# Kernel optimization log

Measured on AMD Instinct MI355X. Metric: run time of the kernel, lower is better.

## Reference

```python
import jax, jax.numpy as jnp
import numpy as np

NUM_HEADS = 16
NUM_GROUPS = 4
NUM_KV_HEADS = NUM_HEADS // NUM_GROUPS  # 4
HEAD_DIM = 64
MAX_DIST = 484


def setup_inputs() -> dict:
    key = jax.random.key(0)
    ks = jax.random.split(key, 8)
    B, S, E, H = 32, 484, 1024, 1024
    kv_dim = HEAD_DIM * NUM_GROUPS  # 256
    s_in = 0.03
    return {
        "query": jax.random.normal(ks[0], (B, S, E), dtype=jnp.float32),
        "key": jax.random.normal(ks[1], (B, S, E), dtype=jnp.float32),
        "value": jax.random.normal(ks[2], (B, S, E), dtype=jnp.float32),
        "Wq": jax.random.normal(ks[3], (E, H), dtype=jnp.float32) * s_in,
        "Wk": jax.random.normal(ks[4], (E, kv_dim), dtype=jnp.float32) * s_in,
        "Wv": jax.random.normal(ks[5], (E, kv_dim), dtype=jnp.float32) * s_in,
        "Wo": jax.random.normal(ks[6], (H, E), dtype=jnp.float32) * s_in,
        "rel_table": jax.random.normal(ks[7], (2 * MAX_DIST - 1, NUM_HEADS), dtype=jnp.float32) * 0.02,
    }


def _rel_bias(rel_table, q_len, k_len):
    # relative position k - q, clipped to [-(MD-1), MD-1], shifted to table index
    rel = jnp.arange(k_len)[None, :] - jnp.arange(q_len)[:, None]
    idx = jnp.clip(rel, -(MAX_DIST - 1), MAX_DIST - 1) + (MAX_DIST - 1)
    bias = rel_table[idx]  # [q, k, heads]
    return jnp.transpose(bias, (2, 0, 1))  # [heads, q, k]


def reference(query, key, value, Wq, Wk, Wv, Wo, rel_table):
    B, Q, _ = query.shape
    K = key.shape[1]
    G, Hkv, D = NUM_GROUPS, NUM_KV_HEADS, HEAD_DIM
    # projections; torch head split: head index = g*Hkv + h
    q = (query @ Wq).reshape(B, Q, G * Hkv, D).transpose(0, 2, 1, 3)
    q = q.reshape(B, G, Hkv, Q, D)  # b g h sq d
    k = (key @ Wk).reshape(B, K, G, D).transpose(0, 2, 1, 3)  # b g sk d
    v = (value @ Wv).reshape(B, K, G, D).transpose(0, 2, 1, 3)  # b g sv d
    scale = jnp.float32(D) ** 0.5
    scores = jnp.einsum('bghqd,bgkd->bghqk', q, k) / scale
    bias = _rel_bias(rel_table, Q, K).reshape(1, G, Hkv, Q, K)
    attn = jax.nn.softmax(scores + bias, axis=-1)
    out = jnp.einsum('bghqk,bgkd->bghqd', attn, v)
    out = out.reshape(B, G * Hkv, Q, D).transpose(0, 2, 1, 3).reshape(B, Q, G * Hkv * D)
    return out @ Wo
```

## Files before the change

kernel.cpp:

```cpp
#include <hip/hip_runtime.h>
#include <hip/hip_bf16.h>

typedef __attribute__((ext_vector_type(8))) short short8;
typedef __attribute__((ext_vector_type(4))) float f32x4;

#define B_  32
#define S_  484
#define E_  1024
#define NH  16
#define SP  512
#define M_  (B_*S_)

static __device__ __forceinline__ ushort f2bf(float f) {
  union { float f; unsigned u; } v; v.f = f;
  unsigned u = v.u;
  return (ushort)((u + 0x7FFFu + ((u >> 16) & 1u)) >> 16);
}

#define GLOAD_LDS16(gp, lp) \
  __builtin_amdgcn_global_load_lds((const __attribute__((address_space(1))) void*)(gp), \
                                   (__attribute__((address_space(3))) void*)(lp), 16, 0, 0)

__global__ __launch_bounds__(256)
void cvt_f32_bf16(const float* __restrict__ x, ushort* __restrict__ y, int n4) {
  int i = blockIdx.x * 256 + threadIdx.x;
  int stride = gridDim.x * 256;
  for (; i < n4; i += stride) {
    float4 v = ((const float4*)x)[i];
    ushort4 h;
    h.x = f2bf(v.x); h.y = f2bf(v.y); h.z = f2bf(v.z); h.w = f2bf(v.w);
    ((ushort4*)y)[i] = h;
  }
}

__global__ __launch_bounds__(256)
void transpose_convert(const float* __restrict__ W, ushort* __restrict__ WT, int K, int N) {
  __shared__ float tile[32][33];
  int k0 = blockIdx.y * 32, n0 = blockIdx.x * 32;
  int tx = threadIdx.x, ty = threadIdx.y;
  for (int i = ty; i < 32; i += 8) tile[i][tx] = W[(size_t)(k0 + i) * N + n0 + tx];
  __syncthreads();
  for (int i = ty; i < 32; i += 8) WT[(size_t)(n0 + i) * K + k0 + tx] = f2bf(tile[tx][i]);
}

template<int EPI, int SWZ>
__global__ __launch_bounds__(256)
void gemm_bt(const ushort* __restrict__ A, const ushort* __restrict__ BT,
             void* __restrict__ Cout, int N, int K, int HN, float oscale) {
  __shared__ alignas(16) ushort sA[2][128 * 32];
  __shared__ alignas(16) ushort sB[2][128 * 32];
  const int tid = threadIdx.x;
  const int lane = tid & 63, w = tid >> 6;
  const int m0 = blockIdx.y * 128, n0 = blockIdx.x * 128;
  const int NK = K >> 5;

  const int srow = w * 32 + (lane >> 2);
  const int scol = (lane & 3) * 8;
  const ushort* gA0 = A  + (size_t)(m0 + srow) * K + scol;
  const ushort* gB0 = BT + (size_t)(n0 + srow) * K + scol;

  const int wr = w >> 1, wc = w & 1;
  const int g4 = lane >> 4, l16 = lane & 15;
  const int aoff = (wr * 64 + l16) * 32 + 8 * g4;
  const int boff = (wc * 64 + l16) * 32 + 8 * g4;

  f32x4 acc[4][4] = {};

  {
    const ushort* ga = gA0; const ushort* gb = gB0;
    GLOAD_LDS16(ga,            &sA[0][(w * 32) * 32]);
    GLOAD_LDS16(ga + 16 * K,   &sA[0][(w * 32 + 16) * 32]);
    GLOAD_LDS16(gb,            &sB[0][(w * 32) * 32]);
    GLOAD_LDS16(gb + 16 * K,   &sB[0][(w * 32 + 16) * 32]);
  }

  for (int kt = 0; kt < NK; ++kt) {
    __syncthreads();
    if (kt + 1 < NK) {
      int nb = (kt + 1) & 1;
      const ushort* ga = gA0 + (kt + 1) * 32;
      const ushort* gb = gB0 + (kt + 1) * 32;
      GLOAD_LDS16(ga,            &sA[nb][(w * 32) * 32]);
      GLOAD_LDS16(ga + 16 * K,   &sA[nb][(w * 32 + 16) * 32]);
      GLOAD_LDS16(gb,            &sB[nb][(w * 32) * 32]);
      GLOAD_LDS16(gb + 16 * K,   &sB[nb][(w * 32 + 16) * 32]);
    }
    const ushort* pa = &sA[kt & 1][aoff];
    const ushort* pb = &sB[kt & 1][boff];
    short8 af[4], bf[4];
#pragma unroll
    for (int i = 0; i < 4; ++i) {
      af[i] = *(const short8*)(pa + i * 16 * 32);
      bf[i] = *(const short8*)(pb + i * 16 * 32);
    }
#pragma unroll
    for (int mi = 0; mi < 4; ++mi)
#pragma unroll
      for (int ni = 0; ni < 4; ++ni)
        acc[mi][ni] = __builtin_amdgcn_mfma_f32_16x16x32_bf16(af[mi], bf[ni], acc[mi][ni], 0, 0, 0);
  }

#pragma unroll
  for (int mi = 0; mi < 4; ++mi) {
#pragma unroll
    for (int ni = 0; ni < 4; ++ni) {
#pragma unroll
      for (int r = 0; r < 4; ++r) {
        int m = m0 + wr * 64 + mi * 16 + g4 * 4 + r;
        int n = n0 + wc * 64 + ni * 16 + l16;
        float vv = acc[mi][ni][r];
        if (EPI == 2) {
          ((float*)Cout)[(size_t)m * N + n] = vv;
        } else {
          int b = m / S_, pos = m % S_;
          if (EPI == 0) {
            int dd = n & 63;
            if (SWZ) dd ^= (pos & 7) << 3;
            ushort hv = f2bf(vv * oscale);
            ((ushort*)Cout)[(((size_t)b * HN + (n >> 6)) * SP + pos) * 64 + dd] = hv;
          } else {
            int pp = pos;
            if (SWZ) pp ^= (n & 3) << 3;
            ushort hv = f2bf(vv);
            ((ushort*)Cout)[(((size_t)b * HN + (n >> 6)) * 64 + (n & 63)) * SP + pp] = hv;
          }
        }
      }
    }
  }
}

__global__ __launch_bounds__(256)
void attn_kernel(const ushort* __restrict__ qp, const ushort* __restrict__ kp,
                 const ushort* __restrict__ vpT, const float* __restrict__ rel,
                 ushort* __restrict__ ao) {
  __shared__ float sBias[1024];
  __shared__ alignas(16) ushort sK[2][32 * 64];
  __shared__ alignas(16) ushort sV[2][64 * 32];
  __shared__ alignas(16) ushort sP[4][16 * 40];
  const int tid = threadIdx.x;
  const int blk = blockIdx.x;
  const int logical = (blk & 7) * 512 + (blk >> 3);
  const int qt = logical & 7, head = (logical >> 3) & 15, b = logical >> 7;
  const int g = head >> 2;
  const float LOG2E = 1.44269504f;
  for (int t = tid; t < 1024; t += 256)
    sBias[t] = (t < 967) ? rel[t * 16 + head] * LOG2E : -1e30f;

  const int lane = tid & 63, w = tid >> 6;
  const int g4 = lane >> 4, l16 = lane & 15;
  const int qw = qt * 64 + w * 16;

  const ushort* qbase = qp + (((size_t)b * NH + head) * SP + qw + l16) * 64;
  short8 qf0 = *(const short8*)(qbase + 8 * g4);
  short8 qf1 = *(const short8*)(qbase + 32 + 8 * g4);

  const ushort* kSrc = kp  + ((size_t)b * 4 + g) * SP * 64 + (tid >> 3) * 64 + (tid & 7) * 8;
  const ushort* vSrc = vpT + ((size_t)b * 4 + g) * 64 * SP + (tid >> 2) * SP + (tid & 3) * 8;

  f32x4 acc[4] = {};
  float ps[4] = {0.f, 0.f, 0.f, 0.f};
  const int ib = l16 - (qw + g4 * 4) + 483;
  ushort* sPw = &sP[w][0];

  const int kswz  = (l16 & 7) << 3;
  const int kOff0 = l16 * 64 + ((8 * g4) ^ kswz);
  const int kOff1 = l16 * 64 + ((32 + 8 * g4) ^ kswz);
  const int vOff  = l16 * 32 + 8 * (g4 ^ (l16 & 3));

  GLOAD_LDS16(kSrc, &sK[0][w * 512]);
  GLOAD_LDS16(vSrc, &sV[0][w * 512]);

  for (int kt = 0; kt < 16; ++kt) {
    __syncthreads();
    if (kt + 1 < 16) {
      GLOAD_LDS16(kSrc + (kt + 1) * 2048, &sK[(kt + 1) & 1][w * 512]);
      GLOAD_LDS16(vSrc + (kt + 1) * 32,   &sV[(kt + 1) & 1][w * 512]);
    }
    const ushort* sk = &sK[kt & 1][0];
    const ushort* sv = &sV[kt & 1][0];
    short8 kf0 = *(const short8*)(sk + kOff0);
    short8 kf1 = *(const short8*)(sk + kOff1);
    short8 kf2 = *(const short8*)(sk + 1024 + kOff0);
    short8 kf3 = *(const short8*)(sk + 1024 + kOff1);
    f32x4 s0 = {}, s1 = {};
    s0 = __builtin_amdgcn_mfma_f32_16x16x32_bf16(qf0, kf0, s0, 0, 0, 0);
    s0 = __builtin_amdgcn_mfma_f32_16x16x32_bf16(qf1, kf1, s0, 0, 0, 0);
    s1 = __builtin_amdgcn_mfma_f32_16x16x32_bf16(qf0, kf2, s1, 0, 0, 0);
    s1 = __builtin_amdgcn_mfma_f32_16x16x32_bf16(qf1, kf3, s1, 0, 0, 0);

    const int k0 = kt * 32;
#pragma unroll
    for (int r = 0; r < 4; ++r) {
      int i0 = ib + k0 - r;
      float p0 = __builtin_amdgcn_exp2f(s0[r] + sBias[i0]);
      float p1 = __builtin_amdgcn_exp2f(s1[r] + sBias[i0 + 16]);
      s0[r] = p0; s1[r] = p1;
      if (kt == 15) {
        p0 = (k0 + l16 < S_) ? p0 : 0.f;
        p1 = (k0 + 16 + l16 < S_) ? p1 : 0.f;
      }
      ps[r] += p0 + p1;
    }
#pragma unroll
    for (int r = 0; r < 4; ++r) {
      int row = g4 * 4 + r;
      sPw[row * 40 + l16]      = f2bf(s0[r]);
      sPw[row * 40 + 16 + l16] = f2bf(s1[r]);
    }
    short8 pf = *(const short8*)(sPw + l16 * 40 + 8 * g4);
#pragma unroll
    for (int nt = 0; nt < 4; ++nt) {
      short8 vf = *(const short8*)(sv + vOff + nt * 512);
      acc[nt] = __builtin_amdgcn_mfma_f32_16x16x32_bf16(pf, vf, acc[nt], 0, 0, 0);
    }
  }

#pragma unroll
  for (int off = 1; off < 16; off <<= 1) {
#pragma unroll
    for (int r = 0; r < 4; ++r) ps[r] += __shfl_xor(ps[r], off, 64);
  }

#pragma unroll
  for (int r = 0; r < 4; ++r) {
    int q_abs = qw + g4 * 4 + r;
    if (q_abs < S_) {
      float inv = 1.f / ps[r];
#pragma unroll
      for (int nt = 0; nt < 4; ++nt) {
        int dd = nt * 16 + l16;
        ao[((size_t)b * S_ + q_abs) * 1024 + head * 64 + dd] = f2bf(acc[nt][r] * inv);
      }
    }
  }
}

extern "C" void kernel_launch(void* const* d_in, const int* in_sizes, int n_in,
                              void* d_out, int out_size, void* d_ws, size_t ws_size,
                              hipStream_t stream) {
  const float* query = (const float*)d_in[0];
  const float* key   = (const float*)d_in[1];
  const float* value = (const float*)d_in[2];
  const float* Wq    = (const float*)d_in[3];
  const float* Wk    = (const float*)d_in[4];
  const float* Wv    = (const float*)d_in[5];
  const float* Wo    = (const float*)d_in[6];
  const float* rel   = (const float*)d_in[7];

  char* ws = (char*)d_ws;
  size_t off = 0;
  auto alloc = [&](size_t bytes) { char* p = ws + off; off += (bytes + 255) & ~(size_t)255; return p; };

  const size_t MEelems = (size_t)M_ * E_;
  ushort* qb  = (ushort*)alloc(MEelems * 2);
  ushort* kb  = (ushort*)alloc(MEelems * 2);
  ushort* vb  = (ushort*)alloc(MEelems * 2);
  ushort* wqT = (ushort*)alloc((size_t)1024 * 1024 * 2);
  ushort* wkT = (ushort*)alloc((size_t)256 * 1024 * 2);
  ushort* wvT = (ushort*)alloc((size_t)256 * 1024 * 2);
  ushort* woT = (ushort*)alloc((size_t)1024 * 1024 * 2);
  ushort* qp  = (ushort*)alloc((size_t)B_ * NH * SP * 64 * 2);
  ushort* kp  = (ushort*)alloc((size_t)B_ * 4 * SP * 64 * 2);
  ushort* vp  = (ushort*)alloc((size_t)B_ * 4 * 64 * SP * 2);
  ushort* ao  = (ushort*)alloc(MEelems * 2);

  const int n4 = (int)(MEelems / 4);
  cvt_f32_bf16<<<2048, 256, 0, stream>>>(query, qb, n4);
  cvt_f32_bf16<<<2048, 256, 0, stream>>>(key,   kb, n4);
  cvt_f32_bf16<<<2048, 256, 0, stream>>>(value, vb, n4);

  transpose_convert<<<dim3(32, 32), dim3(32, 8), 0, stream>>>(Wq, wqT, 1024, 1024);
  transpose_convert<<<dim3(8, 32),  dim3(32, 8), 0, stream>>>(Wk, wkT, 1024, 256);
  transpose_convert<<<dim3(8, 32),  dim3(32, 8), 0, stream>>>(Wv, wvT, 1024, 256);
  transpose_convert<<<dim3(32, 32), dim3(32, 8), 0, stream>>>(Wo, woT, 1024, 1024);

  hipMemsetAsync(qp, 0, (size_t)B_ * NH * SP * 64 * 2 +
                        (size_t)B_ * 4 * SP * 64 * 2 +
                        (size_t)B_ * 4 * 64 * SP * 2, stream);

  const float QSCALE = 0.125f * 1.44269504f;
  gemm_bt<0,0><<<dim3(8, 121), 256, 0, stream>>>(qb, wqT, qp, 1024, 1024, NH, QSCALE);
  gemm_bt<0,1><<<dim3(2, 121), 256, 0, stream>>>(kb, wkT, kp, 256, 1024, 4, 1.0f);
  gemm_bt<1,1><<<dim3(2, 121), 256, 0, stream>>>(vb, wvT, vp, 256, 1024, 4, 1.0f);

  attn_kernel<<<4096, 256, 0, stream>>>(qp, kp, vp, rel, ao);

  gemm_bt<2,0><<<dim3(8, 121), 256, 0, stream>>>(ao, woT, d_out, 1024, 1024, 0, 1.0f);
}
```

Before: 315.3 us.

## Fuse fp32-to-bf16 input conversion into projection GEMMs and pack P stores

Result: slower. 328.8 us (+4.3%).

```diff
diff --git a/kernel.cpp b/kernel.cpp
--- a/kernel.cpp
+++ b/kernel.cpp
@@ -3,6 +3,7 @@
 
 typedef __attribute__((ext_vector_type(8))) short short8;
 typedef __attribute__((ext_vector_type(4))) float f32x4;
+typedef __attribute__((ext_vector_type(4))) unsigned uintx4;
 
 #define B_  32
 #define S_  484
@@ -17,21 +18,15 @@
   return (ushort)((u + 0x7FFFu + ((u >> 16) & 1u)) >> 16);
 }
 
+static __device__ __forceinline__ unsigned cvt_pk_bf16(float lo, float hi) {
+  unsigned r;
+  asm("v_cvt_pk_bf16_f32 %0, %1, %2" : "=v"(r) : "v"(lo), "v"(hi));
+  return r;
+}
+
 #define GLOAD_LDS16(gp, lp) \
   __builtin_amdgcn_global_load_lds((const __attribute__((address_space(1))) void*)(gp), \
                                    (__attribute__((address_space(3))) void*)(lp), 16, 0, 0)
-
-__global__ __launch_bounds__(256)
-void cvt_f32_bf16(const float* __restrict__ x, ushort* __restrict__ y, int n4) {
-  int i = blockIdx.x * 256 + threadIdx.x;
-  int stride = gridDim.x * 256;
-  for (; i < n4; i += stride) {
-    float4 v = ((const float4*)x)[i];
-    ushort4 h;
-    h.x = f2bf(v.x); h.y = f2bf(v.y); h.z = f2bf(v.z); h.w = f2bf(v.w);
-    ((ushort4*)y)[i] = h;
-  }
-}
 
 __global__ __launch_bounds__(256)
 void transpose_convert(const float* __restrict__ W, ushort* __restrict__ WT, int K, int N) {
@@ -43,9 +38,9 @@
   for (int i = ty; i < 32; i += 8) WT[(size_t)(n0 + i) * K + k0 + tx] = f2bf(tile[tx][i]);
 }
 
-template<int EPI, int SWZ>
+template<int EPI, int SWZ, int AF32>
 __global__ __launch_bounds__(256)
-void gemm_bt(const ushort* __restrict__ A, const ushort* __restrict__ BT,
+void gemm_bt(const void* __restrict__ Ain, const ushort* __restrict__ BT,
              void* __restrict__ Cout, int N, int K, int HN, float oscale) {
   __shared__ alignas(16) ushort sA[2][128 * 32];
   __shared__ alignas(16) ushort sB[2][128 * 32];
@@ -56,8 +51,12 @@
 
   const int srow = w * 32 + (lane >> 2);
   const int scol = (lane & 3) * 8;
-  const ushort* gA0 = A  + (size_t)(m0 + srow) * K + scol;
   const ushort* gB0 = BT + (size_t)(n0 + srow) * K + scol;
+
+  const ushort* gA0bf = (const ushort*)Ain + (size_t)(m0 + srow) * K + scol;
+  const int arow = w * 32 + (lane >> 1);
+  const int acol = (lane & 1) * 16;
+  const float* gA0f = (const float*)Ain + (size_t)(m0 + arow) * K + acol;
 
   const int wr = w >> 1, wc = w & 1;
   const int g4 = lane >> 4, l16 = lane & 15;
@@ -65,25 +64,45 @@
   const int boff = (wc * 64 + l16) * 32 + 8 * g4;
 
   f32x4 acc[4][4] = {};
-
-  {
-    const ushort* ga = gA0; const ushort* gb = gB0;
-    GLOAD_LDS16(ga,            &sA[0][(w * 32) * 32]);
-    GLOAD_LDS16(ga + 16 * K,   &sA[0][(w * 32 + 16) * 32]);
-    GLOAD_LDS16(gb,            &sB[0][(w * 32) * 32]);
-    GLOAD_LDS16(gb + 16 * K,   &sB[0][(w * 32 + 16) * 32]);
-  }
+  float4 fA0, fA1, fA2, fA3;
+
+  auto issueA = [&](int kt) {
+    const float4* p = (const float4*)(gA0f + kt * 32);
+    fA0 = p[0]; fA1 = p[1]; fA2 = p[2]; fA3 = p[3];
+  };
+  auto writeA = [&](int buf) {
+    unsigned d0 = cvt_pk_bf16(fA0.x, fA0.y), d1 = cvt_pk_bf16(fA0.z, fA0.w);
+    unsigned d2 = cvt_pk_bf16(fA1.x, fA1.y), d3 = cvt_pk_bf16(fA1.z, fA1.w);
+    unsigned d4 = cvt_pk_bf16(fA2.x, fA2.y), d5 = cvt_pk_bf16(fA2.z, fA2.w);
+    unsigned d6 = cvt_pk_bf16(fA3.x, fA3.y), d7 = cvt_pk_bf16(fA3.z, fA3.w);
+    ushort* dst = &sA[buf][arow * 32 + acol];
+    uintx4 q0 = {d0, d1, d2, d3}, q1 = {d4, d5, d6, d7};
+    *(uintx4*)dst = q0;
+    *(uintx4*)(dst + 8) = q1;
+  };
+
+  if (AF32) issueA(0);
+  else {
+    GLOAD_LDS16(gA0bf,          &sA[0][(w * 32) * 32]);
+    GLOAD_LDS16(gA0bf + 16 * K, &sA[0][(w * 32 + 16) * 32]);
+  }
+  GLOAD_LDS16(gB0,          &sB[0][(w * 32) * 32]);
+  GLOAD_LDS16(gB0 + 16 * K, &sB[0][(w * 32 + 16) * 32]);
+  if (AF32) writeA(0);
 
   for (int kt = 0; kt < NK; ++kt) {
     __syncthreads();
+    const int nb = (kt + 1) & 1;
     if (kt + 1 < NK) {
-      int nb = (kt + 1) & 1;
-      const ushort* ga = gA0 + (kt + 1) * 32;
       const ushort* gb = gB0 + (kt + 1) * 32;
-      GLOAD_LDS16(ga,            &sA[nb][(w * 32) * 32]);
-      GLOAD_LDS16(ga + 16 * K,   &sA[nb][(w * 32 + 16) * 32]);
-      GLOAD_LDS16(gb,            &sB[nb][(w * 32) * 32]);
-      GLOAD_LDS16(gb + 16 * K,   &sB[nb][(w * 32 + 16) * 32]);
+      GLOAD_LDS16(gb,          &sB[nb][(w * 32) * 32]);
+      GLOAD_LDS16(gb + 16 * K, &sB[nb][(w * 32 + 16) * 32]);
+      if (AF32) issueA(kt + 1);
+      else {
+        const ushort* ga = gA0bf + (kt + 1) * 32;
+        GLOAD_LDS16(ga,          &sA[nb][(w * 32) * 32]);
+        GLOAD_LDS16(ga + 16 * K, &sA[nb][(w * 32 + 16) * 32]);
+      }
     }
     const ushort* pa = &sA[kt & 1][aoff];
     const ushort* pb = &sB[kt & 1][boff];
@@ -98,6 +117,7 @@
 #pragma unroll
       for (int ni = 0; ni < 4; ++ni)
         acc[mi][ni] = __builtin_amdgcn_mfma_f32_16x16x32_bf16(af[mi], bf[ni], acc[mi][ni], 0, 0, 0);
+    if (AF32 && kt + 1 < NK) writeA(nb);
   }
 
 #pragma unroll
@@ -119,10 +139,11 @@
             ushort hv = f2bf(vv * oscale);
             ((ushort*)Cout)[(((size_t)b * HN + (n >> 6)) * SP + pos) * 64 + dd] = hv;
           } else {
-            int pp = pos;
-            if (SWZ) pp ^= (n & 3) << 3;
+            int local = pos & 31;
+            int j = (local < 16) ? (2 * local) : (2 * local - 31);
+            int pf_ = (pos & ~31) | (j ^ ((n & 3) << 3));
             ushort hv = f2bf(vv);
-            ((ushort*)Cout)[(((size_t)b * HN + (n >> 6)) * 64 + (n & 63)) * SP + pp] = hv;
+            ((ushort*)Cout)[(((size_t)b * HN + (n >> 6)) * 64 + (n & 63)) * SP + pf_] = hv;
           }
         }
       }
@@ -134,7 +155,7 @@
 void attn_kernel(const ushort* __restrict__ qp, const ushort* __restrict__ kp,
                  const ushort* __restrict__ vpT, const float* __restrict__ rel,
                  ushort* __restrict__ ao) {
-  __shared__ float sBias[1024];
+  __shared__ float sBias[1056];
   __shared__ alignas(16) ushort sK[2][32 * 64];
   __shared__ alignas(16) ushort sV[2][64 * 32];
   __shared__ alignas(16) ushort sP[4][16 * 40];
@@ -144,8 +165,8 @@
   const int qt = logical & 7, head = (logical >> 3) & 15, b = logical >> 7;
   const int g = head >> 2;
   const float LOG2E = 1.44269504f;
-  for (int t = tid; t < 1024; t += 256)
-    sBias[t] = (t < 967) ? rel[t * 16 + head] * LOG2E : -1e30f;
+  for (int t = tid; t < 1056; t += 256)
+    sBias[t] = (t >= 32 && t < 999) ? rel[(t - 32) * 16 + head] * LOG2E : -1e30f;
 
   const int lane = tid & 63, w = tid >> 6;
   const int g4 = lane >> 4, l16 = lane & 15;
@@ -160,7 +181,7 @@
 
   f32x4 acc[4] = {};
   float ps[4] = {0.f, 0.f, 0.f, 0.f};
-  const int ib = l16 - (qw + g4 * 4) + 483;
+  const int ib = l16 - (qw + g4 * 4) + 483 + 32;
   ushort* sPw = &sP[w][0];
 
   const int kswz  = (l16 & 7) << 3;
@@ -195,18 +216,12 @@
       int i0 = ib + k0 - r;
       float p0 = __builtin_amdgcn_exp2f(s0[r] + sBias[i0]);
       float p1 = __builtin_amdgcn_exp2f(s1[r] + sBias[i0 + 16]);
-      s0[r] = p0; s1[r] = p1;
       if (kt == 15) {
         p0 = (k0 + l16 < S_) ? p0 : 0.f;
         p1 = (k0 + 16 + l16 < S_) ? p1 : 0.f;
       }
       ps[r] += p0 + p1;
-    }
-#pragma unroll
-    for (int r = 0; r < 4; ++r) {
-      int row = g4 * 4 + r;
-      sPw[row * 40 + l16]      = f2bf(s0[r]);
-      sPw[row * 40 + 16 + l16] = f2bf(s1[r]);
+      *(unsigned*)(sPw + (g4 * 4 + r) * 40 + 2 * l16) = cvt_pk_bf16(p0, p1);
     }
     short8 pf = *(const short8*)(sPw + l16 * 40 + 8 * g4);
 #pragma unroll
@@ -253,9 +268,6 @@
   auto alloc = [&](size_t bytes) { char* p = ws + off; off += (bytes + 255) & ~(size_t)255; return p; };
 
   const size_t MEelems = (size_t)M_ * E_;
-  ushort* qb  = (ushort*)alloc(MEelems * 2);
-  ushort* kb  = (ushort*)alloc(MEelems * 2);
-  ushort* vb  = (ushort*)alloc(MEelems * 2);
   ushort* wqT = (ushort*)alloc((size_t)1024 * 1024 * 2);
   ushort* wkT = (ushort*)alloc((size_t)256 * 1024 * 2);
   ushort* wvT = (ushort*)alloc((size_t)256 * 1024 * 2);
@@ -265,26 +277,17 @@
   ushort* vp  = (ushort*)alloc((size_t)B_ * 4 * 64 * SP * 2);
   ushort* ao  = (ushort*)alloc(MEelems * 2);
 
-  const int n4 = (int)(MEelems / 4);
-  cvt_f32_bf16<<<2048, 256, 0, stream>>>(query, qb, n4);
-  cvt_f32_bf16<<<2048, 256, 0, stream>>>(key,   kb, n4);
-  cvt_f32_bf16<<<2048, 256, 0, stream>>>(value, vb, n4);
-
   transpose_convert<<<dim3(32, 32), dim3(32, 8), 0, stream>>>(Wq, wqT, 1024, 1024);
   transpose_convert<<<dim3(8, 32),  dim3(32, 8), 0, stream>>>(Wk, wkT, 1024, 256);
   transpose_convert<<<dim3(8, 32),  dim3(32, 8), 0, stream>>>(Wv, wvT, 1024, 256);
   transpose_convert<<<dim3(32, 32), dim3(32, 8), 0, stream>>>(Wo, woT, 1024, 1024);
 
-  hipMemsetAsync(qp, 0, (size_t)B_ * NH * SP * 64 * 2 +
-                        (size_t)B_ * 4 * SP * 64 * 2 +
-                        (size_t)B_ * 4 * 64 * SP * 2, stream);
-
   const float QSCALE = 0.125f * 1.44269504f;
-  gemm_bt<0,0><<<dim3(8, 121), 256, 0, stream>>>(qb, wqT, qp, 1024, 1024, NH, QSCALE);
-  gemm_bt<0,1><<<dim3(2, 121), 256, 0, stream>>>(kb, wkT, kp, 256, 1024, 4, 1.0f);
-  gemm_bt<1,1><<<dim3(2, 121), 256, 0, stream>>>(vb, wvT, vp, 256, 1024, 4, 1.0f);
+  gemm_bt<0,0,1><<<dim3(8, 121), 256, 0, stream>>>(query, wqT, qp, 1024, 1024, NH, QSCALE);
+  gemm_bt<0,1,1><<<dim3(2, 121), 256, 0, stream>>>(key,   wkT, kp, 256, 1024, 4, 1.0f);
+  gemm_bt<1,1,1><<<dim3(2, 121), 256, 0, stream>>>(value, wvT, vp, 256, 1024, 4, 1.0f);
 
   attn_kernel<<<4096, 256, 0, stream>>>(qp, kp, vp, rel, ao);
 
-  gemm_bt<2,0><<<dim3(8, 121), 256, 0, stream>>>(ao, woT, d_out, 1024, 1024, 0, 1.0f);
-}
+  gemm_bt<2,0,0><<<dim3(8, 121), 256, 0, stream>>>(ao, woT, d_out, 1024, 1024, 0, 1.0f);
+}
```
